# Kernel optimization log

Measured on AMD Instinct MI355X. Metric: run time of the kernel, lower is better.

Reference implementation:

```python
import itertools
import jax, jax.numpy as jnp
import numpy as np

G = 128          # grid points per dimension
D_IN = 3         # domain dimension
D_OUT = 16       # codomain dimension
N_QUERY = 1 << 20


def setup_inputs() -> dict:
    key = jax.random.key(0)
    kx, ky = jax.random.split(key)
    # Sorted, non-uniform grid coordinates in [0, 1] per dimension
    base = jnp.linspace(0.0, 1.0, G, dtype=jnp.float32)
    xs0 = base
    xs1 = base ** 1.5            # non-uniform spacing, still sorted
    xs2 = jnp.sqrt(base)         # non-uniform spacing, still sorted
    # Vector-valued samples on the tensor grid
    y = jax.random.normal(ky, (G, G, G, D_OUT), dtype=jnp.float32)
    # Query points, slightly outside [0,1] to exercise clamped extension
    x = jax.random.uniform(kx, (N_QUERY, D_IN), dtype=jnp.float32,
                           minval=-0.1, maxval=1.1)
    return {"x": x, "y": y, "xs0": xs0, "xs1": xs1, "xs2": xs2}


def _interp_linear_clamped(x, y, xs):
    """Multilinear interpolation of grid function y (G,...,G,D) at x (N,d_in),
    clamped extension. Faithful to _grid_interpolate(method='linear',
    extend='clamped')."""
    d_in = len(xs)
    x_min = jnp.stack([g[0] for g in xs])   # (d_in,)
    x_max = jnp.stack([g[-1] for g in xs])  # (d_in,)
    xq = jnp.clip(x, x_min[None], x_max[None])  # clamp to domain

    left, ts = [], []
    for i, g in enumerate(xs):
        n = g.shape[0]
        # index of left grid point: searchsorted right, minus 1
        li = jnp.searchsorted(g, xq[:, i], side="right") - 1
        # points exactly at the upper boundary belong to the last cell
        li = jnp.where(xq[:, i] == g[-1], li - 1, li)
        li = jnp.clip(li, 0, n - 2)  # after clamping all queries are internal
        t = (xq[:, i] - g[li]) / (g[li + 1] - g[li])  # fractional coordinate
        left.append(li)
        ts.append(t)

    # Accumulate over the 2^d_in cell corners
    result = jnp.zeros((x.shape[0], y.shape[-1]), dtype=y.dtype)
    for exponent in itertools.product((0, 1), repeat=d_in):
        c = jnp.ones_like(ts[0])
        for i in range(d_in):
            c = c * (ts[i] if exponent[i] else 1.0 - ts[i])
        idx = tuple(left[i] + exponent[i] for i in range(d_in))
        val = y[idx]  # (N, D_OUT) gather of corner values
        result = result + c[:, None] * val
    return result


def reference(x, y, xs0, xs1, xs2):
    return _interp_linear_clamped(x, y, [xs0, xs1, xs2])
```

## Files before the change

kernel.cpp:

```cpp
#include <hip/hip_runtime.h>

#define G 128
#define D_OUT 16
#define BIN_SHIFT 3
#define NBINS (16 * 16 * 16)
#define NBLK 256
#define QPB 1024
#define MAXCHUNK 5120

typedef float f32x4 __attribute__((ext_vector_type(4)));


__device__ __forceinline__ void stage_grids(const float* __restrict__ xs0,
                                            const float* __restrict__ xs1,
                                            const float* __restrict__ xs2,
                                            float (*sxs)[G], int tid, int nthreads)
{
    for (int i = tid; i < 3 * G; i += nthreads) {
        float v;
        if (i < G)            v = xs0[i];
        else if (i < 2 * G)   v = xs1[i - G];
        else                  v = xs2[i - 2 * G];
        (&sxs[0][0])[i] = v;
    }
}

__device__ __forceinline__ void search1(const float* __restrict__ g, float v,
                                        int& li, float& t)
{
    v = fminf(fmaxf(v, g[0]), g[G - 1]);
    int idx = 0;
    #pragma unroll
    for (int s = 64; s >= 1; s >>= 1) {
        int cand = idx + s;
        if (g[cand] <= v) idx = cand;
    }
    if (idx > G - 2) idx = G - 2;
    li = idx;
    t  = (v - g[idx]) / (g[idx + 1] - g[idx]);
}

__device__ __forceinline__ int bin_of(int li0, int li1, int li2)
{
    return ((li0 >> BIN_SHIFT) << 8) | ((li1 >> BIN_SHIFT) << 4) | (li2 >> BIN_SHIFT);
}

__device__ __forceinline__ unsigned short f2bf(float f)
{
    unsigned int u = __float_as_uint(f);
    u += 0x7FFFu + ((u >> 16) & 1u);
    return (unsigned short)(u >> 16);
}

__device__ __forceinline__ float bf2f(unsigned short h)
{
    return __uint_as_float((unsigned int)h << 16);
}


__global__ __launch_bounds__(256) void hist_kernel(
    const float* __restrict__ x,
    const float* __restrict__ xs0, const float* __restrict__ xs1, const float* __restrict__ xs2,
    unsigned int* __restrict__ counts,
    int n, int qpb)
{
    __shared__ float sxs[3][G];
    __shared__ unsigned int hist[NBINS];
    const int tid = threadIdx.x, blk = blockIdx.x;

    stage_grids(xs0, xs1, xs2, sxs, tid, 256);
    for (int i = tid; i < NBINS; i += 256) hist[i] = 0u;
    __syncthreads();

    const int q0 = blk * qpb, q1 = min(n, q0 + qpb);
    for (int q = q0 + tid; q < q1; q += 256) {
        int li[3]; float t;
        #pragma unroll
        for (int d = 0; d < 3; ++d) search1(sxs[d], x[q * 3 + d], li[d], t);
        atomicAdd(&hist[bin_of(li[0], li[1], li[2])], 1u);
    }
    __syncthreads();

    for (int i = tid; i < NBINS; i += 256)
        counts[(size_t)blk * NBINS + i] = hist[i];
}


__global__ __launch_bounds__(256) void scan_block_kernel(
    const unsigned int* __restrict__ counts,
    unsigned int* __restrict__ offs,
    unsigned int* __restrict__ totals)
{
    __shared__ unsigned int sd[NBLK];
    const int b = blockIdx.x, k = threadIdx.x;
    const unsigned int v = counts[(size_t)k * NBINS + b];
    sd[k] = v;
    __syncthreads();
    for (int off = 1; off < NBLK; off <<= 1) {
        unsigned int t = sd[k];
        unsigned int a = (k >= off) ? sd[k - off] : 0u;
        __syncthreads();
        sd[k] = t + a;
        __syncthreads();
    }
    const unsigned int incl = sd[k];
    offs[(size_t)k * NBINS + b] = incl - v;
    if (k == NBLK - 1) totals[b] = incl;
}


__global__ __launch_bounds__(1024) void scan_totals_kernel(
    const unsigned int* __restrict__ totals,
    unsigned int* __restrict__ bin_base,
    unsigned int* __restrict__ map,
    unsigned int* __restrict__ nchunks)
{
    __shared__ unsigned int sq[1024], sc[1024];
    const int t = threadIdx.x;
    uint4 c = ((const uint4*)totals)[t];
    uint4 h;
    h.x = (c.x + QPB - 1) / QPB;
    h.y = (c.y + QPB - 1) / QPB;
    h.z = (c.z + QPB - 1) / QPB;
    h.w = (c.w + QPB - 1) / QPB;
    const unsigned int sum_q = c.x + c.y + c.z + c.w;
    const unsigned int sum_c = h.x + h.y + h.z + h.w;
    sq[t] = sum_q; sc[t] = sum_c;
    __syncthreads();
    for (int off = 1; off < 1024; off <<= 1) {
        unsigned int vq = sq[t], vc = sc[t];
        unsigned int aq = (t >= off) ? sq[t - off] : 0u;
        unsigned int ac = (t >= off) ? sc[t - off] : 0u;
        __syncthreads();
        sq[t] = vq + aq; sc[t] = vc + ac;
        __syncthreads();
    }
    const unsigned int eq = sq[t] - sum_q;
    const unsigned int ec = sc[t] - sum_c;

    uint4 qb;
    qb.x = eq;
    qb.y = qb.x + c.x;
    qb.z = qb.y + c.y;
    qb.w = qb.z + c.z;
    ((uint4*)bin_base)[t] = qb;
    if (t == 1023) {
        bin_base[NBINS] = sq[1023];
        nchunks[0] = sc[1023];
    }

    unsigned int cb = ec;
    unsigned int hh[4] = { h.x, h.y, h.z, h.w };
    #pragma unroll
    for (int k = 0; k < 4; ++k) {
        const unsigned int binid = ((unsigned int)t << 2) | k;
        for (unsigned int j = 0; j < hh[k]; ++j)
            map[cb + j] = (binid << 8) | j;
        cb += hh[k];
    }
}


__global__ __launch_bounds__(256) void scatter_kernel(
    const float* __restrict__ x,
    const float* __restrict__ xs0, const float* __restrict__ xs1, const float* __restrict__ xs2,
    const unsigned int* __restrict__ offs,
    const unsigned int* __restrict__ bin_base,
    float4* __restrict__ payload,
    int n, int qpb)
{
    __shared__ float sxs[3][G];
    __shared__ unsigned int base[NBINS];
    const int tid = threadIdx.x, blk = blockIdx.x;

    stage_grids(xs0, xs1, xs2, sxs, tid, 256);
    for (int i = tid; i < NBINS; i += 256)
        base[i] = bin_base[i] + offs[(size_t)blk * NBINS + i];
    __syncthreads();

    const int q0 = blk * qpb, q1 = min(n, q0 + qpb);
    for (int q = q0 + tid; q < q1; q += 256) {
        int li0, li1, li2; float t0, t1, t2;
        search1(sxs[0], x[q * 3 + 0], li0, t0);
        search1(sxs[1], x[q * 3 + 1], li1, t1);
        search1(sxs[2], x[q * 3 + 2], li2, t2);
        unsigned int slot = atomicAdd(&base[bin_of(li0, li1, li2)], 1u);
        const unsigned int bits = ((unsigned int)(li0 & 7) << 26)
                                | ((unsigned int)(li1 & 7) << 23)
                                | ((unsigned int)(li2 & 7) << 20)
                                | (unsigned int)q;
        payload[slot] = make_float4(t0, t1, t2, __uint_as_float(bits));
    }
}


__global__ __launch_bounds__(256) void interp_staged_kernel(
    const float4* __restrict__ payload,
    const float* __restrict__ y,
    const unsigned int* __restrict__ bin_base,
    const unsigned int* __restrict__ map,
    const unsigned int* __restrict__ nchunks,
    float* __restrict__ out)
{
    __shared__ unsigned short region[9 * 9 * 9 * D_OUT];
    const int tid = threadIdx.x;

    int bid = blockIdx.x;
    {
        const int chunk = MAXCHUNK >> 3;
        bid = (bid & 7) * chunk + (bid >> 3);
    }
    if ((unsigned int)bid >= nchunks[0]) return;

    const unsigned int info = map[bid];
    const unsigned int bin  = info >> 8;
    const unsigned int chk  = info & 255u;
    const int o0 = (int)((bin >> 8) & 15u) << 3;
    const int o1 = (int)((bin >> 4) & 15u) << 3;
    const int o2 = (int)(bin & 15u) << 3;

    for (int s = tid; s < 81 * 36; s += 256) {
        const int row = s / 36;
        const int f4  = s - row * 36;
        const int l0 = row / 9, l1 = row - l0 * 9;
        const int cc = f4 >> 2, ch = f4 & 3;
        const int g0 = min(o0 + l0, G - 1);
        const int g1 = min(o1 + l1, G - 1);
        const int g2 = min(o2 + cc, G - 1);
        const f32x4 v = *(const f32x4*)(y + ((((g0 << 7) | g1) << 7) | g2) * D_OUT + (ch << 2));
        ushort4 hv;
        hv.x = f2bf(v.x); hv.y = f2bf(v.y); hv.z = f2bf(v.z); hv.w = f2bf(v.w);
        *(ushort4*)&region[((l0 * 9 + l1) * 9 + cc) * D_OUT + (ch << 2)] = hv;
    }
    __syncthreads();

    const unsigned int qs = bin_base[bin] + chk * QPB;
    const unsigned int qe = min(bin_base[bin + 1], qs + QPB);
    const int cg = (tid & 3) << 2;

    for (unsigned int i = qs + (tid >> 2); i < qe; i += 64) {
        const float4 p = payload[i];
        const unsigned int bits = __float_as_uint(p.w);
        const unsigned int q   = bits & 0xFFFFFu;
        const unsigned int lc0 = (bits >> 26) & 7u;
        const unsigned int lc1 = (bits >> 23) & 7u;
        const unsigned int lc2 = (bits >> 20) & 7u;

        const float t0 = p.x, t1 = p.y, t2 = p.z;
        const float u0 = 1.f - t0, u1 = 1.f - t1, u2 = 1.f - t2;

        const int base = (int)((lc0 * 9u + lc1) * 9u + lc2) * D_OUT + cg;
        const int d2 = D_OUT, d1 = 9 * D_OUT, d0 = 81 * D_OUT;

        const ushort4 h000 = *(const ushort4*)&region[base];
        const ushort4 h001 = *(const ushort4*)&region[base + d2];
        const ushort4 h010 = *(const ushort4*)&region[base + d1];
        const ushort4 h011 = *(const ushort4*)&region[base + d1 + d2];
        const ushort4 h100 = *(const ushort4*)&region[base + d0];
        const ushort4 h101 = *(const ushort4*)&region[base + d0 + d2];
        const ushort4 h110 = *(const ushort4*)&region[base + d0 + d1];
        const ushort4 h111 = *(const ushort4*)&region[base + d0 + d1 + d2];

        const float w000 = u0 * u1 * u2, w001 = u0 * u1 * t2;
        const float w010 = u0 * t1 * u2, w011 = u0 * t1 * t2;
        const float w100 = t0 * u1 * u2, w101 = t0 * u1 * t2;
        const float w110 = t0 * t1 * u2, w111 = t0 * t1 * t2;

        f32x4 acc;
        #pragma unroll
        for (int k = 0; k < 4; ++k) {
            const unsigned short* a000 = &h000.x;
            acc[k] = w000 * bf2f((&h000.x)[k]) + w001 * bf2f((&h001.x)[k])
                   + w010 * bf2f((&h010.x)[k]) + w011 * bf2f((&h011.x)[k])
                   + w100 * bf2f((&h100.x)[k]) + w101 * bf2f((&h101.x)[k])
                   + w110 * bf2f((&h110.x)[k]) + w111 * bf2f((&h111.x)[k]);
            (void)a000;
        }

        __builtin_nontemporal_store(acc, (f32x4*)(out + (size_t)q * D_OUT + cg));
    }
}


__global__ __launch_bounds__(256) void interp3d_kernel(
    const float* __restrict__ x, const float* __restrict__ y,
    const float* __restrict__ xs0, const float* __restrict__ xs1, const float* __restrict__ xs2,
    float* __restrict__ out, int nquery)
{
    __shared__ float sxs[3][G];
    stage_grids(xs0, xs1, xs2, sxs, threadIdx.x, 256);
    __syncthreads();

    const int q = blockIdx.x * 64 + (threadIdx.x >> 2);
    if (q >= nquery) return;
    const int cg = (threadIdx.x & 3) * 4;

    int li[3]; float t[3];
    #pragma unroll
    for (int d = 0; d < 3; ++d) search1(sxs[d], x[q * 3 + d], li[d], t[d]);

    const float w0[3] = { 1.f - t[0], 1.f - t[1], 1.f - t[2] };
    const float w1[3] = { t[0], t[1], t[2] };

    float4 acc = make_float4(0.f, 0.f, 0.f, 0.f);
    #pragma unroll
    for (int e = 0; e < 8; ++e) {
        const int e0 = (e >> 2) & 1, e1 = (e >> 1) & 1, e2 = e & 1;
        const float w = (e0 ? w1[0] : w0[0]) * (e1 ? w1[1] : w0[1]) * (e2 ? w1[2] : w0[2]);
        const int idx = ((li[0] + e0) * G + (li[1] + e1)) * G + (li[2] + e2);
        const float4 v = *(const float4*)(y + (size_t)idx * D_OUT + cg);
        acc.x += w * v.x; acc.y += w * v.y; acc.z += w * v.z; acc.w += w * v.w;
    }
    *(float4*)(out + (size_t)q * D_OUT + cg) = acc;
}

extern "C" void kernel_launch(void* const* d_in, const int* in_sizes, int n_in,
                              void* d_out, int out_size, void* d_ws, size_t ws_size,
                              hipStream_t stream) {
    const float* x   = (const float*)d_in[0];
    const float* y   = (const float*)d_in[1];
    const float* xs0 = (const float*)d_in[2];
    const float* xs1 = (const float*)d_in[3];
    const float* xs2 = (const float*)d_in[4];
    float* out = (float*)d_out;

    const int nquery = in_sizes[0] / 3;

    const size_t counts_elems = (size_t)NBLK * NBINS;
    const size_t need = (size_t)nquery * sizeof(float4)
                      + (2 * counts_elems + NBINS + (NBINS + 1) + MAXCHUNK + 16) * sizeof(unsigned int);
    if (ws_size < need || nquery > (1 << 20)) {
        const int blocks = (nquery + 63) / 64;
        hipLaunchKernelGGL(interp3d_kernel, dim3(blocks), dim3(256), 0, stream,
                           x, y, xs0, xs1, xs2, out, nquery);
        return;
    }

    float4*       payload  = (float4*)d_ws;
    unsigned int* counts   = (unsigned int*)(payload + nquery);
    unsigned int* offs     = counts + counts_elems;
    unsigned int* totals   = offs + counts_elems;
    unsigned int* bin_base = totals + NBINS;
    unsigned int* map      = bin_base + (NBINS + 1);
    unsigned int* nchunks  = map + MAXCHUNK;

    const int qpb = (nquery + NBLK - 1) / NBLK;

    hipLaunchKernelGGL(hist_kernel, dim3(NBLK), dim3(256), 0, stream,
                       x, xs0, xs1, xs2, counts, nquery, qpb);
    hipLaunchKernelGGL(scan_block_kernel, dim3(NBINS), dim3(NBLK), 0, stream,
                       counts, offs, totals);
    hipLaunchKernelGGL(scan_totals_kernel, dim3(1), dim3(1024), 0, stream,
                       totals, bin_base, map, nchunks);
    hipLaunchKernelGGL(scatter_kernel, dim3(NBLK), dim3(256), 0, stream,
                       x, xs0, xs1, xs2, offs, bin_base, payload, nquery, qpb);
    hipLaunchKernelGGL(interp_staged_kernel, dim3(MAXCHUNK), dim3(256), 0, stream,
                       payload, y, bin_base, map, nchunks, out);
}
```

Baseline: 105.1 us.

## Use persistent blocks with atomic work queue for staged interpolation

Replaces the one-block-per-chunk launch of the interpolation kernel with a fixed set of persistent 512-thread blocks. Each block pulls chunk indices from a global atomic counter, which the scan kernel resets to zero. This is meant to cut the cost of launching and retiring blocks, including the early-exit blocks beyond nchunks, and to balance uneven chunk sizes. It adds an atomic and two block barriers per chunk. The LDS tile staging is also serialized with the compute inside each block, so staging no longer overlaps with other blocks' compute unless several blocks share a CU.

```diff
diff --git a/kernel.cpp b/kernel.cpp
--- a/kernel.cpp
+++ b/kernel.cpp
@@ -7,6 +7,7 @@
 #define NBLK 256
 #define QPB 1024
 #define MAXCHUNK 5120
+#define PBLK 1024
 
 typedef float f32x4 __attribute__((ext_vector_type(4)));
 
@@ -113,10 +114,12 @@
     const unsigned int* __restrict__ totals,
     unsigned int* __restrict__ bin_base,
     unsigned int* __restrict__ map,
-    unsigned int* __restrict__ nchunks)
+    unsigned int* __restrict__ nchunks,
+    unsigned int* __restrict__ counter)
 {
     __shared__ unsigned int sq[1024], sc[1024];
     const int t = threadIdx.x;
+    if (t == 0) counter[0] = 0u;
     uint4 c = ((const uint4*)totals)[t];
     uint4 h;
     h.x = (c.x + QPB - 1) / QPB;
@@ -194,90 +197,92 @@
 }
 
 
-__global__ __launch_bounds__(256) void interp_staged_kernel(
+__global__ __launch_bounds__(512, 8) void interp_staged_kernel(
     const float4* __restrict__ payload,
     const float* __restrict__ y,
     const unsigned int* __restrict__ bin_base,
     const unsigned int* __restrict__ map,
     const unsigned int* __restrict__ nchunks,
+    unsigned int* __restrict__ counter,
     float* __restrict__ out)
 {
     __shared__ unsigned short region[9 * 9 * 9 * D_OUT];
+    __shared__ unsigned int s_cur;
     const int tid = threadIdx.x;
-
-    int bid = blockIdx.x;
-    {
-        const int chunk = MAXCHUNK >> 3;
-        bid = (bid & 7) * chunk + (bid >> 3);
-    }
-    if ((unsigned int)bid >= nchunks[0]) return;
-
-    const unsigned int info = map[bid];
-    const unsigned int bin  = info >> 8;
-    const unsigned int chk  = info & 255u;
-    const int o0 = (int)((bin >> 8) & 15u) << 3;
-    const int o1 = (int)((bin >> 4) & 15u) << 3;
-    const int o2 = (int)(bin & 15u) << 3;
-
-    for (int s = tid; s < 81 * 36; s += 256) {
-        const int row = s / 36;
-        const int f4  = s - row * 36;
-        const int l0 = row / 9, l1 = row - l0 * 9;
-        const int cc = f4 >> 2, ch = f4 & 3;
-        const int g0 = min(o0 + l0, G - 1);
-        const int g1 = min(o1 + l1, G - 1);
-        const int g2 = min(o2 + cc, G - 1);
-        const f32x4 v = *(const f32x4*)(y + ((((g0 << 7) | g1) << 7) | g2) * D_OUT + (ch << 2));
-        ushort4 hv;
-        hv.x = f2bf(v.x); hv.y = f2bf(v.y); hv.z = f2bf(v.z); hv.w = f2bf(v.w);
-        *(ushort4*)&region[((l0 * 9 + l1) * 9 + cc) * D_OUT + (ch << 2)] = hv;
-    }
-    __syncthreads();
-
-    const unsigned int qs = bin_base[bin] + chk * QPB;
-    const unsigned int qe = min(bin_base[bin + 1], qs + QPB);
+    const unsigned int nch = nchunks[0];
     const int cg = (tid & 3) << 2;
 
-    for (unsigned int i = qs + (tid >> 2); i < qe; i += 64) {
-        const float4 p = payload[i];
-        const unsigned int bits = __float_as_uint(p.w);
-        const unsigned int q   = bits & 0xFFFFFu;
-        const unsigned int lc0 = (bits >> 26) & 7u;
-        const unsigned int lc1 = (bits >> 23) & 7u;
-        const unsigned int lc2 = (bits >> 20) & 7u;
-
-        const float t0 = p.x, t1 = p.y, t2 = p.z;
-        const float u0 = 1.f - t0, u1 = 1.f - t1, u2 = 1.f - t2;
-
-        const int base = (int)((lc0 * 9u + lc1) * 9u + lc2) * D_OUT + cg;
-        const int d2 = D_OUT, d1 = 9 * D_OUT, d0 = 81 * D_OUT;
-
-        const ushort4 h000 = *(const ushort4*)&region[base];
-        const ushort4 h001 = *(const ushort4*)&region[base + d2];
-        const ushort4 h010 = *(const ushort4*)&region[base + d1];
-        const ushort4 h011 = *(const ushort4*)&region[base + d1 + d2];
-        const ushort4 h100 = *(const ushort4*)&region[base + d0];
-        const ushort4 h101 = *(const ushort4*)&region[base + d0 + d2];
-        const ushort4 h110 = *(const ushort4*)&region[base + d0 + d1];
-        const ushort4 h111 = *(const ushort4*)&region[base + d0 + d1 + d2];
-
-        const float w000 = u0 * u1 * u2, w001 = u0 * u1 * t2;
-        const float w010 = u0 * t1 * u2, w011 = u0 * t1 * t2;
-        const float w100 = t0 * u1 * u2, w101 = t0 * u1 * t2;
-        const float w110 = t0 * t1 * u2, w111 = t0 * t1 * t2;
-
-        f32x4 acc;
-        #pragma unroll
-        for (int k = 0; k < 4; ++k) {
-            const unsigned short* a000 = &h000.x;
-            acc[k] = w000 * bf2f((&h000.x)[k]) + w001 * bf2f((&h001.x)[k])
-                   + w010 * bf2f((&h010.x)[k]) + w011 * bf2f((&h011.x)[k])
-                   + w100 * bf2f((&h100.x)[k]) + w101 * bf2f((&h101.x)[k])
-                   + w110 * bf2f((&h110.x)[k]) + w111 * bf2f((&h111.x)[k]);
-            (void)a000;
+    for (;;) {
+        if (tid == 0) s_cur = atomicAdd(counter, 1u);
+        __syncthreads();
+        const unsigned int bid = s_cur;
+        if (bid >= nch) break;
+
+        const unsigned int info = map[bid];
+        const unsigned int bin  = info >> 8;
+        const unsigned int chk  = info & 255u;
+        const int o0 = (int)((bin >> 8) & 15u) << 3;
+        const int o1 = (int)((bin >> 4) & 15u) << 3;
+        const int o2 = (int)(bin & 15u) << 3;
+
+        for (int s = tid; s < 81 * 36; s += 512) {
+            const int row = s / 36;
+            const int f4  = s - row * 36;
+            const int l0 = row / 9, l1 = row - l0 * 9;
+            const int cc = f4 >> 2, ch = f4 & 3;
+            const int g0 = min(o0 + l0, G - 1);
+            const int g1 = min(o1 + l1, G - 1);
+            const int g2 = min(o2 + cc, G - 1);
+            const f32x4 v = *(const f32x4*)(y + ((((g0 << 7) | g1) << 7) | g2) * D_OUT + (ch << 2));
+            ushort4 hv;
+            hv.x = f2bf(v.x); hv.y = f2bf(v.y); hv.z = f2bf(v.z); hv.w = f2bf(v.w);
+            *(ushort4*)&region[((l0 * 9 + l1) * 9 + cc) * D_OUT + (ch << 2)] = hv;
         }
-
-        __builtin_nontemporal_store(acc, (f32x4*)(out + (size_t)q * D_OUT + cg));
+        __syncthreads();
+
+        const unsigned int qs = bin_base[bin] + chk * QPB;
+        const unsigned int qe = min(bin_base[bin + 1], qs + QPB);
+
+        for (unsigned int i = qs + (tid >> 2); i < qe; i += 128) {
+            const float4 p = payload[i];
+            const unsigned int bits = __float_as_uint(p.w);
+            const unsigned int q   = bits & 0xFFFFFu;
+            const unsigned int lc0 = (bits >> 26) & 7u;
+            const unsigned int lc1 = (bits >> 23) & 7u;
+            const unsigned int lc2 = (bits >> 20) & 7u;
+
+            const float t0 = p.x, t1 = p.y, t2 = p.z;
+            const float u0 = 1.f - t0, u1 = 1.f - t1, u2 = 1.f - t2;
+
+            const int base = (int)((lc0 * 9u + lc1) * 9u + lc2) * D_OUT + cg;
+            const int d2 = D_OUT, d1 = 9 * D_OUT, d0 = 81 * D_OUT;
+
+            const ushort4 h000 = *(const ushort4*)&region[base];
+            const ushort4 h001 = *(const ushort4*)&region[base + d2];
+            const ushort4 h010 = *(const ushort4*)&region[base + d1];
+            const ushort4 h011 = *(const ushort4*)&region[base + d1 + d2];
+            const ushort4 h100 = *(const ushort4*)&region[base + d0];
+            const ushort4 h101 = *(const ushort4*)&region[base + d0 + d2];
+            const ushort4 h110 = *(const ushort4*)&region[base + d0 + d1];
+            const ushort4 h111 = *(const ushort4*)&region[base + d0 + d1 + d2];
+
+            const float w000 = u0 * u1 * u2, w001 = u0 * u1 * t2;
+            const float w010 = u0 * t1 * u2, w011 = u0 * t1 * t2;
+            const float w100 = t0 * u1 * u2, w101 = t0 * u1 * t2;
+            const float w110 = t0 * t1 * u2, w111 = t0 * t1 * t2;
+
+            f32x4 acc;
+            #pragma unroll
+            for (int k = 0; k < 4; ++k) {
+                acc[k] = w000 * bf2f((&h000.x)[k]) + w001 * bf2f((&h001.x)[k])
+                       + w010 * bf2f((&h010.x)[k]) + w011 * bf2f((&h011.x)[k])
+                       + w100 * bf2f((&h100.x)[k]) + w101 * bf2f((&h101.x)[k])
+                       + w110 * bf2f((&h110.x)[k]) + w111 * bf2f((&h111.x)[k]);
+            }
+
+            __builtin_nontemporal_store(acc, (f32x4*)(out + (size_t)q * D_OUT + cg));
+        }
+        __syncthreads();
     }
 }
 
@@ -343,6 +348,7 @@
     unsigned int* bin_base = totals + NBINS;
     unsigned int* map      = bin_base + (NBINS + 1);
     unsigned int* nchunks  = map + MAXCHUNK;
+    unsigned int* counter  = nchunks + 1;
 
     const int qpb = (nquery + NBLK - 1) / NBLK;
 
@@ -351,9 +357,9 @@
     hipLaunchKernelGGL(scan_block_kernel, dim3(NBINS), dim3(NBLK), 0, stream,
                        counts, offs, totals);
     hipLaunchKernelGGL(scan_totals_kernel, dim3(1), dim3(1024), 0, stream,
-                       totals, bin_base, map, nchunks);
+                       totals, bin_base, map, nchunks, counter);
     hipLaunchKernelGGL(scatter_kernel, dim3(NBLK), dim3(256), 0, stream,
                        x, xs0, xs1, xs2, offs, bin_base, payload, nquery, qpb);
-    hipLaunchKernelGGL(interp_staged_kernel, dim3(MAXCHUNK), dim3(256), 0, stream,
-                       payload, y, bin_base, map, nchunks, out);
-}
+    hipLaunchKernelGGL(interp_staged_kernel, dim3(PBLK), dim3(512), 0, stream,
+                       payload, y, bin_base, map, nchunks, counter, out);
+}
```

Result: slower. 130.1 us (+23.8%).
